# Performance work log

Hardware: AMD Instinct MI355X
Metric: run time of the kernel (lower is better)

## Reference

```python
import jax, jax.numpy as jnp
import numpy as np

NU, NI = 100000, 50000      # global embedding table sizes
U, I = 50000, 20000         # nodes in this subgraph
E = 400000                  # edges per direction
HID, H = 512, 8
D = HID // H                # out_feats per head = 64
NEG_SLOPE = 0.2


def setup_inputs() -> dict:
    key = jax.random.key(0)
    ks = jax.random.split(key, 16)
    s = 1.0 / np.sqrt(HID)
    a = 1.0 / np.sqrt(D)
    return {
        'u_gid': jax.random.randint(ks[0], (U,), 0, NU),
        'i_gid': jax.random.randint(ks[1], (I,), 0, NI),
        'src_u': jax.random.randint(ks[2], (E,), 0, U),
        'dst_i': jax.random.randint(ks[3], (E,), 0, I),
        'user_emb': jax.random.normal(ks[4], (NU, HID), jnp.float32) * 0.02,
        'item_emb': jax.random.normal(ks[5], (NI, HID), jnp.float32) * 0.02,
        # 'interact' (user -> item) GATConv params
        'W_ui': jax.random.normal(ks[6], (HID, HID), jnp.float32) * s,
        'al_ui': jax.random.normal(ks[7], (H, D), jnp.float32) * a,
        'ar_ui': jax.random.normal(ks[8], (H, D), jnp.float32) * a,
        'b_ui': jnp.zeros((HID,), jnp.float32),
        # 'interact_rev' (item -> user) GATConv params
        'W_iu': jax.random.normal(ks[9], (HID, HID), jnp.float32) * s,
        'al_iu': jax.random.normal(ks[10], (H, D), jnp.float32) * a,
        'ar_iu': jax.random.normal(ks[11], (H, D), jnp.float32) * a,
        'b_iu': jnp.zeros((HID,), jnp.float32),
    }


def gat_conv(h_src, h_dst, src, dst, W, attn_l, attn_r, bias, n_dst):
    """DGL GATConv (eval mode, allow_zero_in_degree): [n_dst, H, D]."""
    fs = (h_src @ W).reshape(-1, H, D)            # [Ns,H,D]
    fd = (h_dst @ W).reshape(-1, H, D)            # [Nd,H,D]
    el = jnp.sum(fs * attn_l, axis=-1)            # [Ns,H]
    er = jnp.sum(fd * attn_r, axis=-1)            # [Nd,H]
    e = jax.nn.leaky_relu(el[src] + er[dst], NEG_SLOPE)   # [E,H]
    # segment softmax over incoming edges of each destination
    emax = jax.ops.segment_max(e, dst, num_segments=n_dst)[dst]
    ex = jnp.exp(e - emax)                        # [E,H]
    denom = jax.ops.segment_sum(ex, dst, num_segments=n_dst)[dst]
    alpha = ex / denom                            # [E,H]
    msg = fs[src] * alpha[:, :, None]             # [E,H,D]
    out = jax.ops.segment_sum(msg, dst, num_segments=n_dst)  # zero for isolated dst
    return out + bias.reshape(1, H, D)


def reference(u_gid, i_gid, src_u, dst_i, user_emb, item_emb,
              W_ui, al_ui, ar_ui, b_ui, W_iu, al_iu, ar_iu, b_iu):
    h_u0 = user_emb[u_gid]                        # [U,HID]
    h_i0 = item_emb[i_gid]                        # [I,HID]
    # 'interact': user -> item
    h_item = gat_conv(h_u0, h_i0, src_u, dst_i, W_ui, al_ui, ar_ui, b_ui, I)
    # 'interact_rev': item -> user (reversed edges)
    h_user = gat_conv(h_i0, h_u0, dst_i, src_u, W_iu, al_iu, ar_iu, b_iu, U)
    h_user = h_user.reshape(U, HID)
    h_item = h_item.reshape(I, HID)
    item_mean = jnp.mean(h_item, axis=0, keepdims=True)        # [1,HID]
    item_expand = jnp.broadcast_to(item_mean, (U, HID))
    return jnp.concatenate([h_user, item_expand], axis=1)      # [U, 2*HID]
```

## Files before the change

### kernel.cpp

```cpp
#include <hip/hip_runtime.h>
#include <hip/hip_bf16.h>
#include <stdint.h>

#define U_NODES 50000
#define I_NODES 20000
#define N_NODES 70000
#define M_PAD   70016
#define E_EDGES 400000
#define HID     512

typedef __attribute__((ext_vector_type(8))) short short8;
typedef __attribute__((ext_vector_type(4))) float floatx4;

static __device__ __forceinline__ uint16_t f2b(float f) {
    uint32_t x = __float_as_uint(f);
    x += 0x7fffu + ((x >> 16) & 1u);
    return (uint16_t)(x >> 16);
}
static __device__ __forceinline__ float b2f(short u) {
    return __uint_as_float(((uint32_t)(uint16_t)u) << 16);
}

__global__ void gather_cast(const int* __restrict__ u_gid, const int* __restrict__ i_gid,
                            const float* __restrict__ user_emb, const float* __restrict__ item_emb,
                            uint16_t* __restrict__ Xb)
{
    int t = blockIdx.x * 256 + threadIdx.x;
    int n = t >> 7;
    int j = (t & 127) << 2;
    uint2 o;
    if (n < N_NODES) {
        const float* src = (n < U_NODES) ? (user_emb + (size_t)u_gid[n] * HID)
                                         : (item_emb + (size_t)i_gid[n - U_NODES] * HID);
        float4 v = *(const float4*)(src + j);
        o.x = (uint32_t)f2b(v.x) | ((uint32_t)f2b(v.y) << 16);
        o.y = (uint32_t)f2b(v.z) | ((uint32_t)f2b(v.w) << 16);
    } else { o.x = 0u; o.y = 0u; }
    *(uint2*)(Xb + (size_t)n * HID + j) = o;
}

__global__ void prep_w(const float* __restrict__ Wui, const float* __restrict__ Wiu,
                       uint16_t* __restrict__ Wt)
{
    int t = blockIdx.x * 256 + threadIdx.x;
    int n = t >> 9, k = t & 511;
    float v = (n < 512) ? Wui[k * 512 + n] : Wiu[k * 512 + (n - 512)];
    Wt[(size_t)n * 512 + k] = f2b(v);
}

__global__ __launch_bounds__(256) void gemm_bf16(const uint16_t* __restrict__ Xb,
                                                 const uint16_t* __restrict__ Wt,
                                                 uint16_t* __restrict__ F)
{
    __shared__ __align__(16) uint16_t As[128 * 32];
    __shared__ __align__(16) uint16_t Bs[128 * 32];
    const int tid = threadIdx.x;
    const int wave = tid >> 6, lane = tid & 63;
    const int m0 = (blockIdx.x >> 3) * 128;
    const int n0 = (blockIdx.x & 7) * 128;
    const int wm = (wave & 1) * 64;
    const int wn = (wave >> 1) * 64;

    const int c0 = wave * 64 + lane;
    const int c1 = c0 + 256;
    const uint16_t* gA0 = Xb + (size_t)(m0 + (c0 >> 2)) * HID + (c0 & 3) * 8;
    const uint16_t* gA1 = Xb + (size_t)(m0 + (c1 >> 2)) * HID + (c1 & 3) * 8;
    const uint16_t* gB0 = Wt + (size_t)(n0 + (c0 >> 2)) * HID + (c0 & 3) * 8;
    const uint16_t* gB1 = Wt + (size_t)(n0 + (c1 >> 2)) * HID + (c1 & 3) * 8;
    uint16_t* lA0 = As + wave * 512;
    uint16_t* lA1 = As + 2048 + wave * 512;
    uint16_t* lB0 = Bs + wave * 512;
    uint16_t* lB1 = Bs + 2048 + wave * 512;

    floatx4 zero = {0.f, 0.f, 0.f, 0.f};
    floatx4 acc[4][4];
    #pragma unroll
    for (int a = 0; a < 4; ++a)
        #pragma unroll
        for (int b = 0; b < 4; ++b) acc[a][b] = zero;

    const int r = lane & 15, quad = lane >> 4;

    for (int k0 = 0; k0 < HID; k0 += 32) {
        __syncthreads();
        __builtin_amdgcn_global_load_lds((const __attribute__((address_space(1))) void*)(gA0 + k0),
                                         (__attribute__((address_space(3))) void*)lA0, 16, 0, 0);
        __builtin_amdgcn_global_load_lds((const __attribute__((address_space(1))) void*)(gA1 + k0),
                                         (__attribute__((address_space(3))) void*)lA1, 16, 0, 0);
        __builtin_amdgcn_global_load_lds((const __attribute__((address_space(1))) void*)(gB0 + k0),
                                         (__attribute__((address_space(3))) void*)lB0, 16, 0, 0);
        __builtin_amdgcn_global_load_lds((const __attribute__((address_space(1))) void*)(gB1 + k0),
                                         (__attribute__((address_space(3))) void*)lB1, 16, 0, 0);
        __syncthreads();
        short8 af[4], bf[4];
        #pragma unroll
        for (int tm = 0; tm < 4; ++tm)
            af[tm] = *(const short8*)&As[(wm + tm * 16 + r) * 32 + quad * 8];
        #pragma unroll
        for (int tn = 0; tn < 4; ++tn)
            bf[tn] = *(const short8*)&Bs[(wn + tn * 16 + r) * 32 + quad * 8];
        #pragma unroll
        for (int tm = 0; tm < 4; ++tm)
            #pragma unroll
            for (int tn = 0; tn < 4; ++tn)
                acc[tm][tn] = __builtin_amdgcn_mfma_f32_16x16x32_bf16(af[tm], bf[tn], acc[tm][tn], 0, 0, 0);
    }
    #pragma unroll
    for (int tm = 0; tm < 4; ++tm) {
        #pragma unroll
        for (int rr = 0; rr < 4; ++rr) {
            int row = m0 + wm + tm * 16 + quad * 4 + rr;
            if (row < N_NODES) {
                #pragma unroll
                for (int tn = 0; tn < 4; ++tn) {
                    int col = n0 + wn + tn * 16 + r;
                    F[(size_t)row * 1024 + col] = f2b(acc[tm][tn][rr]);
                }
            }
        }
    }
}

__global__ void elr_kernel(const uint16_t* __restrict__ F,
                           const float* __restrict__ al_ui, const float* __restrict__ ar_ui,
                           const float* __restrict__ al_iu, const float* __restrict__ ar_iu,
                           float* __restrict__ ELui, float* __restrict__ ERui,
                           float* __restrict__ ELiu, float* __restrict__ ERiu)
{
    int n = blockIdx.x * 4 + (threadIdx.x >> 6);
    if (n >= N_NODES) return;
    int lane = threadIdx.x & 63;
    int base = lane * 8;
    short8 a = *(const short8*)&F[(size_t)n * 1024 + base];
    short8 b = *(const short8*)&F[(size_t)n * 1024 + 512 + base];
    float s0 = 0.f, s1 = 0.f, s2 = 0.f, s3 = 0.f;
    #pragma unroll
    for (int j = 0; j < 8; ++j) {
        float fa = b2f(a[j]), fb = b2f(b[j]);
        s0 += fa * al_ui[base + j];
        s1 += fa * ar_ui[base + j];
        s2 += fb * al_iu[base + j];
        s3 += fb * ar_iu[base + j];
    }
    #pragma unroll
    for (int d = 1; d < 8; d <<= 1) {
        s0 += __shfl_xor(s0, d, 8);
        s1 += __shfl_xor(s1, d, 8);
        s2 += __shfl_xor(s2, d, 8);
        s3 += __shfl_xor(s3, d, 8);
    }
    if ((lane & 7) == 0) {
        int h = lane >> 3;
        ELui[n * 8 + h] = s0;
        ERui[n * 8 + h] = s1;
        ELiu[n * 8 + h] = s2;
        ERiu[n * 8 + h] = s3;
    }
}

__global__ void hist_kernel(const int* __restrict__ src_u, const int* __restrict__ dst_i,
                            int* __restrict__ counts_i, int* __restrict__ counts_u)
{
    int e = blockIdx.x * 256 + threadIdx.x;
    if (e >= E_EDGES) return;
    atomicAdd(&counts_i[dst_i[e]], 1);
    atomicAdd(&counts_u[src_u[e]], 1);
}

__global__ __launch_bounds__(1024) void scan_kernel(const int* __restrict__ counts_i,
                                                    const int* __restrict__ counts_u,
                                                    int* __restrict__ offs_i, int* __restrict__ cur_i,
                                                    int* __restrict__ offs_u, int* __restrict__ cur_u)
{
    const int* counts; int n; int* offs; int* cur;
    if (blockIdx.x == 0) { counts = counts_i; n = I_NODES; offs = offs_i; cur = cur_i; }
    else                 { counts = counts_u; n = U_NODES; offs = offs_u; cur = cur_u; }
    __shared__ int wsum[16];
    int tid = threadIdx.x, lane = tid & 63, w = tid >> 6;
    int carry = 0;
    for (int base = 0; base < n; base += 1024) {
        int i = base + tid;
        int v = (i < n) ? counts[i] : 0;
        int x = v;
        #pragma unroll
        for (int d = 1; d < 64; d <<= 1) {
            int y = __shfl_up(x, d, 64);
            if (lane >= d) x += y;
        }
        if (lane == 63) wsum[w] = x;
        __syncthreads();
        if (w == 0) {
            int s = (lane < 16) ? wsum[lane] : 0;
            #pragma unroll
            for (int d = 1; d < 16; d <<= 1) {
                int y = __shfl_up(s, d, 16);
                if ((lane & 15) >= d) s += y;
            }
            if (lane < 16) wsum[lane] = s;
        }
        __syncthreads();
        int wexcl = (w == 0) ? 0 : wsum[w - 1];
        int excl = carry + wexcl + (x - v);
        if (i < n) { offs[i] = excl; cur[i] = excl; }
        int tot = wsum[15];
        __syncthreads();
        carry += tot;
    }
    if (tid == 0) offs[n] = carry;
}

__global__ void scatter_kernel(const int* __restrict__ src_u, const int* __restrict__ dst_i,
                               int* __restrict__ cur_i, int* __restrict__ cur_u,
                               int* __restrict__ sorted_ui, int* __restrict__ sorted_iu,
                               const float* __restrict__ ELui, const float* __restrict__ ERui,
                               const float* __restrict__ ELiu, const float* __restrict__ ERiu,
                               float* __restrict__ ex_ui, float* __restrict__ ex_iu)
{
    int e = blockIdx.x * 256 + threadIdx.x;
    if (e >= E_EDGES) return;
    int s = src_u[e], d = dst_i[e];
    int dn = U_NODES + d;
    int p = atomicAdd(&cur_i[d], 1);
    int q = atomicAdd(&cur_u[s], 1);
    sorted_ui[p] = s;
    sorted_iu[q] = dn;
    #pragma unroll
    for (int h = 0; h < 8; ++h) {
        float e1 = ELui[s * 8 + h] + ERui[dn * 8 + h];
        e1 = (e1 >= 0.f) ? e1 : 0.2f * e1;
        ex_ui[(size_t)p * 8 + h] = __expf(e1);
        float e2 = ELiu[dn * 8 + h] + ERiu[s * 8 + h];
        e2 = (e2 >= 0.f) ? e2 : 0.2f * e2;
        ex_iu[(size_t)q * 8 + h] = __expf(e2);
    }
}

#define IBLK ((I_NODES + 3) / 4)
#define UBLK ((U_NODES + 3) / 4)
__global__ __launch_bounds__(256) void agg3_kernel(
    const int* __restrict__ offs_i, const int* __restrict__ sorted_ui, const float* __restrict__ ex_ui,
    const int* __restrict__ offs_u, const int* __restrict__ sorted_iu, const float* __restrict__ ex_iu,
    const uint16_t* __restrict__ F, const float* __restrict__ b_iu,
    float* __restrict__ out, float* __restrict__ itemF)
{
    int bid = blockIdx.x;
    int w = threadIdx.x >> 6, lane = threadIdx.x & 63;
    bool item_mode = bid < IBLK;
    const int* offs; const int* srcs; const float* ex; int dst, colbase, n_dst;
    if (item_mode) { offs = offs_i; srcs = sorted_ui; ex = ex_ui; dst = bid * 4 + w;          colbase = 0;   n_dst = I_NODES; }
    else           { offs = offs_u; srcs = sorted_iu; ex = ex_iu; dst = (bid - IBLK) * 4 + w; colbase = 512; n_dst = U_NODES; }
    if (dst >= n_dst) return;
    int h = lane >> 3;
    int j0 = offs[dst], j1 = offs[dst + 1];

    float den = 0.f;
    float acc[8] = {0.f, 0.f, 0.f, 0.f, 0.f, 0.f, 0.f, 0.f};
    const int fb = colbase + lane * 8;
    int j = j0;
    for (; j + 8 <= j1; j += 8) {
        int s[8]; float wt[8]; short8 f[8];
        #pragma unroll
        for (int i = 0; i < 8; ++i) s[i] = srcs[j + i];
        #pragma unroll
        for (int i = 0; i < 8; ++i) wt[i] = ex[(size_t)(j + i) * 8 + h];
        #pragma unroll
        for (int i = 0; i < 8; ++i) f[i] = *(const short8*)&F[(size_t)s[i] * 1024 + fb];
        #pragma unroll
        for (int i = 0; i < 8; ++i) {
            den += wt[i];
            #pragma unroll
            for (int q = 0; q < 8; ++q) acc[q] += wt[i] * b2f(f[i][q]);
        }
    }
    for (; j + 4 <= j1; j += 4) {
        int s[4]; float wt[4]; short8 f[4];
        #pragma unroll
        for (int i = 0; i < 4; ++i) s[i] = srcs[j + i];
        #pragma unroll
        for (int i = 0; i < 4; ++i) wt[i] = ex[(size_t)(j + i) * 8 + h];
        #pragma unroll
        for (int i = 0; i < 4; ++i) f[i] = *(const short8*)&F[(size_t)s[i] * 1024 + fb];
        #pragma unroll
        for (int i = 0; i < 4; ++i) {
            den += wt[i];
            #pragma unroll
            for (int q = 0; q < 8; ++q) acc[q] += wt[i] * b2f(f[i][q]);
        }
    }
    for (; j < j1; ++j) {
        int s0 = srcs[j];
        float w0 = ex[(size_t)j * 8 + h];
        short8 f0 = *(const short8*)&F[(size_t)s0 * 1024 + fb];
        den += w0;
        #pragma unroll
        for (int q = 0; q < 8; ++q) acc[q] += w0 * b2f(f0[q]);
    }
    float inv = (j1 > j0) ? (1.f / den) : 0.f;
    #pragma unroll
    for (int q = 0; q < 8; ++q) acc[q] *= inv;

    int col = lane * 8;
    if (item_mode) {
        float* o = itemF + (size_t)dst * 512 + col;
        float4 v0 = {acc[0], acc[1], acc[2], acc[3]};
        float4 v1 = {acc[4], acc[5], acc[6], acc[7]};
        *(float4*)(o + 0) = v0;
        *(float4*)(o + 4) = v1;
    } else {
        float* o = out + (size_t)dst * 1024 + col;
        float4 v0 = {acc[0] + b_iu[col + 0], acc[1] + b_iu[col + 1],
                     acc[2] + b_iu[col + 2], acc[3] + b_iu[col + 3]};
        float4 v1 = {acc[4] + b_iu[col + 4], acc[5] + b_iu[col + 5],
                     acc[6] + b_iu[col + 6], acc[7] + b_iu[col + 7]};
        *(float4*)(o + 0) = v0;
        *(float4*)(o + 4) = v1;
    }
}

__global__ void item_reduce(const float* __restrict__ itemF, float* __restrict__ partial2)
{
    int b = blockIdx.x;
    int t = threadIdx.x;
    int cg = (t & 127) * 4;
    int rp = t >> 7;
    float4 s = {0.f, 0.f, 0.f, 0.f};
    int r0 = b * 500;
    for (int r = r0 + rp; r < r0 + 500; r += 2) {
        float4 v = *(const float4*)&itemF[(size_t)r * 512 + cg];
        s.x += v.x; s.y += v.y; s.z += v.z; s.w += v.w;
    }
    *(float4*)&partial2[(size_t)(b * 2 + rp) * 512 + cg] = s;
}

__global__ void meanvec_kernel(const float* __restrict__ partial2, const float* __restrict__ b_ui,
                               float* __restrict__ mean_vec)
{
    int c = threadIdx.x;
    float s = 0.f;
    for (int p = 0; p < 80; ++p) s += partial2[p * 512 + c];
    mean_vec[c] = s * (1.0f / (float)I_NODES) + b_ui[c];
}

__global__ void bcast_kernel(const float* __restrict__ mean_vec, float* __restrict__ out)
{
    int t = blockIdx.x * 256 + threadIdx.x;
    int u = t >> 7, q = t & 127;
    float4 v = ((const float4*)mean_vec)[q];
    *(float4*)(out + (size_t)u * 1024 + 512 + q * 4) = v;
}

extern "C" void kernel_launch(void* const* d_in, const int* in_sizes, int n_in,
                              void* d_out, int out_size, void* d_ws, size_t ws_size,
                              hipStream_t stream)
{
    const int*   u_gid    = (const int*)d_in[0];
    const int*   i_gid    = (const int*)d_in[1];
    const int*   src_u    = (const int*)d_in[2];
    const int*   dst_i    = (const int*)d_in[3];
    const float* user_emb = (const float*)d_in[4];
    const float* item_emb = (const float*)d_in[5];
    const float* W_ui     = (const float*)d_in[6];
    const float* al_ui    = (const float*)d_in[7];
    const float* ar_ui    = (const float*)d_in[8];
    const float* b_ui     = (const float*)d_in[9];
    const float* W_iu     = (const float*)d_in[10];
    const float* al_iu    = (const float*)d_in[11];
    const float* ar_iu    = (const float*)d_in[12];
    const float* b_iu     = (const float*)d_in[13];
    float* out = (float*)d_out;

    char* ws = (char*)d_ws;
    size_t off = 0;
    auto alloc = [&](size_t bytes) -> void* {
        void* p = ws + off;
        off = (off + bytes + 255) & ~(size_t)255;
        return p;
    };
    uint16_t* Xb   = (uint16_t*)alloc((size_t)M_PAD * 512 * 2);
    uint16_t* Wt   = (uint16_t*)alloc((size_t)1024 * 512 * 2);
    uint16_t* F    = (uint16_t*)alloc((size_t)M_PAD * 1024 * 2);
    float* ELui    = (float*)alloc((size_t)N_NODES * 8 * 4);
    float* ERui    = (float*)alloc((size_t)N_NODES * 8 * 4);
    float* ELiu    = (float*)alloc((size_t)N_NODES * 8 * 4);
    float* ERiu    = (float*)alloc((size_t)N_NODES * 8 * 4);
    int* offs_i    = (int*)alloc((size_t)(I_NODES + 1) * 4);
    int* cur_i     = (int*)alloc((size_t)I_NODES * 4);
    int* offs_u    = (int*)alloc((size_t)(U_NODES + 1) * 4);
    int* cur_u     = (int*)alloc((size_t)U_NODES * 4);
    int* sorted_ui = (int*)alloc((size_t)E_EDGES * 4);
    int* sorted_iu = (int*)alloc((size_t)E_EDGES * 4);
    float* ex_ui   = (float*)alloc((size_t)E_EDGES * 8 * 4);
    float* ex_iu   = (float*)alloc((size_t)E_EDGES * 8 * 4);
    float* itemF   = (float*)alloc((size_t)I_NODES * 512 * 4);
    float* partial2= (float*)alloc((size_t)80 * 512 * 4);
    char* zptr = ws + off;
    int*   counts_i = (int*)alloc((size_t)I_NODES * 4);
    int*   counts_u = (int*)alloc((size_t)U_NODES * 4);
    size_t zbytes = (size_t)((ws + off) - zptr);
    float* mean_vec = (float*)alloc(512 * 4);
    (void)ws_size; (void)in_sizes; (void)n_in; (void)out_size;

    hipMemsetAsync(zptr, 0, zbytes, stream);
    prep_w<<<2048, 256, 0, stream>>>(W_ui, W_iu, Wt);
    gather_cast<<<M_PAD * 128 / 256, 256, 0, stream>>>(u_gid, i_gid, user_emb, item_emb, Xb);
    gemm_bf16<<<(M_PAD / 128) * 8, 256, 0, stream>>>(Xb, Wt, F);
    elr_kernel<<<(N_NODES + 3) / 4, 256, 0, stream>>>(F, al_ui, ar_ui, al_iu, ar_iu,
                                                      ELui, ERui, ELiu, ERiu);
    hist_kernel<<<(E_EDGES + 255) / 256, 256, 0, stream>>>(src_u, dst_i, counts_i, counts_u);
    scan_kernel<<<2, 1024, 0, stream>>>(counts_i, counts_u, offs_i, cur_i, offs_u, cur_u);
    scatter_kernel<<<(E_EDGES + 255) / 256, 256, 0, stream>>>(src_u, dst_i, cur_i, cur_u,
                                                              sorted_ui, sorted_iu,
                                                              ELui, ERui, ELiu, ERiu,
                                                              ex_ui, ex_iu);
    agg3_kernel<<<IBLK + UBLK, 256, 0, stream>>>(offs_i, sorted_ui, ex_ui,
                                                 offs_u, sorted_iu, ex_iu,
                                                 F, b_iu, out, itemF);
    item_reduce<<<40, 256, 0, stream>>>(itemF, partial2);
    meanvec_kernel<<<1, 512, 0, stream>>>(partial2, b_ui, mean_vec);
    bcast_kernel<<<U_NODES * 128 / 256, 256, 0, stream>>>(mean_vec, out);
}
```

Measured before the change: 905.9 us.

## Fuse attention-logit dot products into GEMM epilogue; widen K tile with swizzled LDS

The separate elr_kernel is removed. The per-head el/er dot products are now computed in the GEMM epilogue from fp32 accumulators, using 16-lane shuffles, so F no longer has to be re-read. The GEMM K-step goes from 32 to 64 with an XOR-swizzled LDS layout to cut bank conflicts. Blocks are also remapped (x*547+ii) so that tiles sharing X rows run on different XCDs or in a cache-friendly order. El/er now come from unrounded fp32 values rather than bf16, which shifts numerics slightly, and LDS use doubles.

```diff
diff --git a/kernel.cpp b/kernel.cpp
--- a/kernel.cpp
+++ b/kernel.cpp
@@ -50,27 +50,37 @@
 
 __global__ __launch_bounds__(256) void gemm_bf16(const uint16_t* __restrict__ Xb,
                                                  const uint16_t* __restrict__ Wt,
-                                                 uint16_t* __restrict__ F)
-{
-    __shared__ __align__(16) uint16_t As[128 * 32];
-    __shared__ __align__(16) uint16_t Bs[128 * 32];
+                                                 const float* __restrict__ al_ui, const float* __restrict__ ar_ui,
+                                                 const float* __restrict__ al_iu, const float* __restrict__ ar_iu,
+                                                 uint16_t* __restrict__ F,
+                                                 float* __restrict__ ELui, float* __restrict__ ERui,
+                                                 float* __restrict__ ELiu, float* __restrict__ ERiu)
+{
+    __shared__ __align__(16) uint16_t As[128 * 64];
+    __shared__ __align__(16) uint16_t Bs[128 * 64];
     const int tid = threadIdx.x;
     const int wave = tid >> 6, lane = tid & 63;
-    const int m0 = (blockIdx.x >> 3) * 128;
-    const int n0 = (blockIdx.x & 7) * 128;
+
+    int bid = blockIdx.x;
+    int x = bid & 7, ii = bid >> 3;
+    int L = x * 547 + ii;
+    const int m0 = (L >> 3) * 128;
+    const int n0 = (L & 7) * 128;
     const int wm = (wave & 1) * 64;
     const int wn = (wave >> 1) * 64;
 
-    const int c0 = wave * 64 + lane;
-    const int c1 = c0 + 256;
-    const uint16_t* gA0 = Xb + (size_t)(m0 + (c0 >> 2)) * HID + (c0 & 3) * 8;
-    const uint16_t* gA1 = Xb + (size_t)(m0 + (c1 >> 2)) * HID + (c1 & 3) * 8;
-    const uint16_t* gB0 = Wt + (size_t)(n0 + (c0 >> 2)) * HID + (c0 & 3) * 8;
-    const uint16_t* gB1 = Wt + (size_t)(n0 + (c1 >> 2)) * HID + (c1 & 3) * 8;
-    uint16_t* lA0 = As + wave * 512;
-    uint16_t* lA1 = As + 2048 + wave * 512;
-    uint16_t* lB0 = Bs + wave * 512;
-    uint16_t* lB1 = Bs + 2048 + wave * 512;
+    const int rl = lane >> 3;
+    const int sg8 = ((lane & 7) ^ rl) * 8;
+    const uint16_t* gA[4]; const uint16_t* gB[4];
+    uint16_t* lA[4]; uint16_t* lB[4];
+    #pragma unroll
+    for (int l = 0; l < 4; ++l) {
+        int c = wave * 4 + l;
+        gA[l] = Xb + (size_t)(m0 + c * 8 + rl) * HID + sg8;
+        gB[l] = Wt + (size_t)(n0 + c * 8 + rl) * HID + sg8;
+        lA[l] = As + c * 512;
+        lB[l] = Bs + c * 512;
+    }
 
     floatx4 zero = {0.f, 0.f, 0.f, 0.f};
     floatx4 acc[4][4];
@@ -80,31 +90,41 @@
         for (int b = 0; b < 4; ++b) acc[a][b] = zero;
 
     const int r = lane & 15, quad = lane >> 4;
-
-    for (int k0 = 0; k0 < HID; k0 += 32) {
+    const int rx = r & 7;
+
+    for (int k0 = 0; k0 < HID; k0 += 64) {
         __syncthreads();
-        __builtin_amdgcn_global_load_lds((const __attribute__((address_space(1))) void*)(gA0 + k0),
-                                         (__attribute__((address_space(3))) void*)lA0, 16, 0, 0);
-        __builtin_amdgcn_global_load_lds((const __attribute__((address_space(1))) void*)(gA1 + k0),
-                                         (__attribute__((address_space(3))) void*)lA1, 16, 0, 0);
-        __builtin_amdgcn_global_load_lds((const __attribute__((address_space(1))) void*)(gB0 + k0),
-                                         (__attribute__((address_space(3))) void*)lB0, 16, 0, 0);
-        __builtin_amdgcn_global_load_lds((const __attribute__((address_space(1))) void*)(gB1 + k0),
-                                         (__attribute__((address_space(3))) void*)lB1, 16, 0, 0);
+        #pragma unroll
+        for (int l = 0; l < 4; ++l) {
+            __builtin_amdgcn_global_load_lds((const __attribute__((address_space(1))) void*)(gA[l] + k0),
+                                             (__attribute__((address_space(3))) void*)lA[l], 16, 0, 0);
+            __builtin_amdgcn_global_load_lds((const __attribute__((address_space(1))) void*)(gB[l] + k0),
+                                             (__attribute__((address_space(3))) void*)lB[l], 16, 0, 0);
+        }
         __syncthreads();
-        short8 af[4], bf[4];
-        #pragma unroll
-        for (int tm = 0; tm < 4; ++tm)
-            af[tm] = *(const short8*)&As[(wm + tm * 16 + r) * 32 + quad * 8];
-        #pragma unroll
-        for (int tn = 0; tn < 4; ++tn)
-            bf[tn] = *(const short8*)&Bs[(wn + tn * 16 + r) * 32 + quad * 8];
-        #pragma unroll
-        for (int tm = 0; tm < 4; ++tm)
-            #pragma unroll
-            for (int tn = 0; tn < 4; ++tn)
-                acc[tm][tn] = __builtin_amdgcn_mfma_f32_16x16x32_bf16(af[tm], bf[tn], acc[tm][tn], 0, 0, 0);
-    }
+        #pragma unroll
+        for (int ks = 0; ks < 2; ++ks) {
+            short8 af[4], bf[4];
+            #pragma unroll
+            for (int tm = 0; tm < 4; ++tm) {
+                int row = wm + tm * 16 + r;
+                int sl = (ks * 4 + quad) ^ rx;
+                af[tm] = *(const short8*)&As[row * 64 + sl * 8];
+            }
+            #pragma unroll
+            for (int tn = 0; tn < 4; ++tn) {
+                int row = wn + tn * 16 + r;
+                int sl = (ks * 4 + quad) ^ rx;
+                bf[tn] = *(const short8*)&Bs[row * 64 + sl * 8];
+            }
+            #pragma unroll
+            for (int tm = 0; tm < 4; ++tm)
+                #pragma unroll
+                for (int tn = 0; tn < 4; ++tn)
+                    acc[tm][tn] = __builtin_amdgcn_mfma_f32_16x16x32_bf16(af[tm], bf[tn], acc[tm][tn], 0, 0, 0);
+        }
+    }
+
     #pragma unroll
     for (int tm = 0; tm < 4; ++tm) {
         #pragma unroll
@@ -119,42 +139,43 @@
             }
         }
     }
-}
-
-__global__ void elr_kernel(const uint16_t* __restrict__ F,
-                           const float* __restrict__ al_ui, const float* __restrict__ ar_ui,
-                           const float* __restrict__ al_iu, const float* __restrict__ ar_iu,
-                           float* __restrict__ ELui, float* __restrict__ ERui,
-                           float* __restrict__ ELiu, float* __restrict__ ERiu)
-{
-    int n = blockIdx.x * 4 + (threadIdx.x >> 6);
-    if (n >= N_NODES) return;
-    int lane = threadIdx.x & 63;
-    int base = lane * 8;
-    short8 a = *(const short8*)&F[(size_t)n * 1024 + base];
-    short8 b = *(const short8*)&F[(size_t)n * 1024 + 512 + base];
-    float s0 = 0.f, s1 = 0.f, s2 = 0.f, s3 = 0.f;
-    #pragma unroll
-    for (int j = 0; j < 8; ++j) {
-        float fa = b2f(a[j]), fb = b2f(b[j]);
-        s0 += fa * al_ui[base + j];
-        s1 += fa * ar_ui[base + j];
-        s2 += fb * al_iu[base + j];
-        s3 += fb * ar_iu[base + j];
-    }
-    #pragma unroll
-    for (int d = 1; d < 8; d <<= 1) {
-        s0 += __shfl_xor(s0, d, 8);
-        s1 += __shfl_xor(s1, d, 8);
-        s2 += __shfl_xor(s2, d, 8);
-        s3 += __shfl_xor(s3, d, 8);
-    }
-    if ((lane & 7) == 0) {
-        int h = lane >> 3;
-        ELui[n * 8 + h] = s0;
-        ERui[n * 8 + h] = s1;
-        ELiu[n * 8 + h] = s2;
-        ERiu[n * 8 + h] = s3;
+
+    int colh = n0 + wn;
+    bool is_ui = colh < 512;
+    int h = (colh & 511) >> 6;
+    const float* alv = is_ui ? al_ui : al_iu;
+    const float* arv = is_ui ? ar_ui : ar_iu;
+    float* ELp = is_ui ? ELui : ELiu;
+    float* ERp = is_ui ? ERui : ERiu;
+    float al4[4], ar4[4];
+    #pragma unroll
+    for (int tn = 0; tn < 4; ++tn) {
+        al4[tn] = alv[h * 64 + tn * 16 + r];
+        ar4[tn] = arv[h * 64 + tn * 16 + r];
+    }
+    #pragma unroll
+    for (int tm = 0; tm < 4; ++tm) {
+        #pragma unroll
+        for (int rr = 0; rr < 4; ++rr) {
+            float sl = 0.f, sr = 0.f;
+            #pragma unroll
+            for (int tn = 0; tn < 4; ++tn) {
+                sl += acc[tm][tn][rr] * al4[tn];
+                sr += acc[tm][tn][rr] * ar4[tn];
+            }
+            #pragma unroll
+            for (int d = 1; d < 16; d <<= 1) {
+                sl += __shfl_xor(sl, d);
+                sr += __shfl_xor(sr, d);
+            }
+            if (r == 0) {
+                int row = m0 + wm + tm * 16 + quad * 4 + rr;
+                if (row < N_NODES) {
+                    ELp[row * 8 + h] = sl;
+                    ERp[row * 8 + h] = sr;
+                }
+            }
+        }
     }
 }
 
@@ -403,9 +424,8 @@
     hipMemsetAsync(zptr, 0, zbytes, stream);
     prep_w<<<2048, 256, 0, stream>>>(W_ui, W_iu, Wt);
     gather_cast<<<M_PAD * 128 / 256, 256, 0, stream>>>(u_gid, i_gid, user_emb, item_emb, Xb);
-    gemm_bf16<<<(M_PAD / 128) * 8, 256, 0, stream>>>(Xb, Wt, F);
-    elr_kernel<<<(N_NODES + 3) / 4, 256, 0, stream>>>(F, al_ui, ar_ui, al_iu, ar_iu,
-                                                      ELui, ERui, ELiu, ERiu);
+    gemm_bf16<<<(M_PAD / 128) * 8, 256, 0, stream>>>(Xb, Wt, al_ui, ar_ui, al_iu, ar_iu,
+                                                     F, ELui, ERui, ELiu, ERiu);
     hist_kernel<<<(E_EDGES + 255) / 256, 256, 0, stream>>>(src_u, dst_i, counts_i, counts_u);
     scan_kernel<<<2, 1024, 0, stream>>>(counts_i, counts_u, offs_i, cur_i, offs_u, cur_u);
     scatter_kernel<<<(E_EDGES + 255) / 256, 256, 0, stream>>>(src_u, dst_i, cur_i, cur_u,
```

New measurement: 918.7 us. About the same (+1.4%).
